# Optimization experiments

Measured on AMD Instinct MI355X. Metric: run time of the kernel, lower is better.

The kernel has to match this reference:

```python
import jax, jax.numpy as jnp
import numpy as np

N = 50000
E = 800000
D_IN = 128
D_HID = 256


def setup_inputs() -> dict:
    key = jax.random.key(0)
    ks = jax.random.split(key, 9)
    x = jax.random.normal(ks[0], (N, D_IN), dtype=jnp.float32)
    edge_index = jax.random.randint(ks[1], (2, E), 0, N, dtype=jnp.int64)
    edge_weight = jax.random.uniform(ks[2], (E,), dtype=jnp.float32)
    # GCNConv params (lin: y = x @ W.T, plus bias added after aggregation)
    W1 = jax.random.normal(ks[3], (D_HID, D_IN), dtype=jnp.float32) / np.sqrt(D_IN)
    b1 = jnp.zeros((D_HID,), dtype=jnp.float32)
    W2 = jax.random.normal(ks[4], (D_IN, D_HID), dtype=jnp.float32) / np.sqrt(D_HID)
    b2 = jnp.zeros((D_IN,), dtype=jnp.float32)
    gamma = jnp.ones((D_IN,), dtype=jnp.float32)
    beta = jnp.zeros((D_IN,), dtype=jnp.float32)
    return {"x": x, "edge_index": edge_index, "edge_weight": edge_weight,
            "W1": W1, "b1": b1, "W2": W2, "b2": b2,
            "gamma": gamma, "beta": beta}


def _gcn_norm(edge_index, edge_weight, n_nodes):
    # add self loops with weight 1.0 (PyG gcn_norm default)
    loop = jnp.arange(n_nodes, dtype=edge_index.dtype)
    src = jnp.concatenate([edge_index[0], loop])
    dst = jnp.concatenate([edge_index[1], loop])
    w = jnp.concatenate([edge_weight, jnp.ones((n_nodes,), edge_weight.dtype)])
    # symmetric normalization: deg over target index
    deg = jax.ops.segment_sum(w, dst, num_segments=n_nodes)
    dinv = jnp.where(deg > 0, jax.lax.rsqrt(deg), 0.0)
    norm = dinv[src] * w * dinv[dst]
    return src, dst, norm


def _gcn_conv(x, src, dst, norm, W, b, n_nodes):
    h = x @ W.T                                    # [N, out]
    msg = h[src] * norm[:, None]                   # gather + scale [E+N, out]
    out = jax.ops.segment_sum(msg, dst, num_segments=n_nodes)
    return out + b


def reference(x, edge_index, edge_weight, W1, b1, W2, b2, gamma, beta):
    n_nodes = x.shape[0]
    src, dst, norm = _gcn_norm(edge_index, edge_weight, n_nodes)
    h = _gcn_conv(x, src, dst, norm, W1, b1, n_nodes)
    h = jax.nn.relu(h)
    h = _gcn_conv(h, src, dst, norm, W2, b2, n_nodes)
    # LayerNorm over last dim
    mu = jnp.mean(h, axis=-1, keepdims=True)
    var = jnp.mean(jnp.square(h - mu), axis=-1, keepdims=True)
    h = (h - mu) * jax.lax.rsqrt(var + 1e-5) * gamma + beta
    return h
```

## Files before the change

### kernel.cpp

```cpp
#include <hip/hip_runtime.h>

typedef unsigned short ushort_t;
typedef __attribute__((ext_vector_type(8))) short short8;
typedef __attribute__((ext_vector_type(4))) float float4v;

#define MAXDEG 48
#define CSTRIDE 16

__device__ inline float b2f(ushort_t u) {
    unsigned x = ((unsigned)u) << 16;
    return __builtin_bit_cast(float, x);
}
__device__ inline ushort_t f2b(float f) {
    unsigned x = __builtin_bit_cast(unsigned, f);
    unsigned r = (x + 0x7fffu + ((x >> 16) & 1u)) >> 16;
    return (ushort_t)r;
}

__device__ inline void load_edge(const int* __restrict__ ei, int e, int E,
                                 int& s, int& d) {
    int ec = min(e, E - 1);
    int2 c64 = ((const int2*)ei)[ec];
    unsigned long long m = __ballot(c64.y != 0);
    if (m != 0ull) {
        s = ei[ec];
        d = ei[(size_t)E + ec];
    } else {
        s = c64.x;
        d = ((const int2*)ei)[(size_t)E + ec].x;
    }
}


__global__ __launch_bounds__(256) void k_mega(const int* __restrict__ ei,
                                              const float* __restrict__ w,
                                              const float* __restrict__ x,
                                              const float* __restrict__ W1,
                                              const float* __restrict__ W2,
                                              unsigned* packed,
                                              unsigned* __restrict__ edata,
                                              ushort_t* __restrict__ xb,
                                              ushort_t* __restrict__ W1b,
                                              ushort_t* __restrict__ W2b,
                                              int E, int Nn, int gE, int gX) {
    int b = blockIdx.x;
    if (b < gE) {
        int e = b * 256 + threadIdx.x;
        int s, d;
        load_edge(ei, e, E, s, d);
        if (e < E) {
            if ((unsigned)s < (unsigned)Nn && (unsigned)d < (unsigned)Nn) {
                float wv = w[e];
                unsigned fx = (unsigned)(wv * 65536.0f + 0.5f);
                unsigned old = atomicAdd(packed + (size_t)d * CSTRIDE,
                                         (1u << 22) | fx);
                int r = (int)(old >> 22);
                if (r < MAXDEG) {
                    unsigned wq = (unsigned)(wv * 32768.0f + 0.5f);
                    wq = min(wq, 32767u);
                    edata[(size_t)d * MAXDEG + r] = ((unsigned)s << 15) | wq;
                }
            }
        }
    } else if (b < gE + gX) {
        int i = (b - gE) * 256 + threadIdx.x;
        if (i < Nn * 32) {
            float4v v = ((const float4v*)x)[i];
            ushort4 o;
            o.x = f2b(v[0]); o.y = f2b(v[1]); o.z = f2b(v[2]); o.w = f2b(v[3]);
            ((ushort4*)xb)[i] = o;
        }
    } else {
        int i = (b - gE - gX) * 256 + threadIdx.x;
        if (i < 32768) W1b[i] = f2b(W1[i]);
        else if (i < 65536) W2b[i - 32768] = f2b(W2[i - 32768]);
    }
}


__global__ __launch_bounds__(256) void k_dinv(const unsigned* __restrict__ packed,
                                              float* __restrict__ dinv, int Nn) {
    int i = blockIdx.x * 256 + threadIdx.x;
    if (i < Nn) {
        float wsum = (float)(packed[(size_t)i * CSTRIDE] & 0x3FFFFFu) * (1.0f / 65536.0f);
        dinv[i] = rsqrtf(1.0f + wsum);
    }
}


__device__ inline void agg_edges(const ushort_t* __restrict__ src,
                                 const unsigned* __restrict__ ed, int n,
                                 const float* __restrict__ dinv,
                                 int hl, int p, float* a) {
    int i = 0;
    for (; i + 15 < n; i += 16) {
        unsigned e2[8];
#pragma unroll
        for (int j = 0; j < 8; ++j) e2[j] = ed[i + p + 2 * j];
        ushort4 q[8];
        float nw[8];
#pragma unroll
        for (int j = 0; j < 8; ++j) {
            int sN = (int)(e2[j] >> 15);
            q[j] = ((const ushort4*)(src + (size_t)sN * 128))[hl];
            nw[j] = dinv[sN] * (float)(e2[j] & 0x7FFFu) * (1.0f / 32768.0f);
        }
#pragma unroll
        for (int j = 0; j < 8; ++j) {
            a[0] += b2f(q[j].x) * nw[j]; a[1] += b2f(q[j].y) * nw[j];
            a[2] += b2f(q[j].z) * nw[j]; a[3] += b2f(q[j].w) * nw[j];
        }
    }
    for (; i + 7 < n; i += 8) {
        unsigned e2[4];
#pragma unroll
        for (int j = 0; j < 4; ++j) e2[j] = ed[i + p + 2 * j];
        ushort4 q[4];
        float nw[4];
#pragma unroll
        for (int j = 0; j < 4; ++j) {
            int sN = (int)(e2[j] >> 15);
            q[j] = ((const ushort4*)(src + (size_t)sN * 128))[hl];
            nw[j] = dinv[sN] * (float)(e2[j] & 0x7FFFu) * (1.0f / 32768.0f);
        }
#pragma unroll
        for (int j = 0; j < 4; ++j) {
            a[0] += b2f(q[j].x) * nw[j]; a[1] += b2f(q[j].y) * nw[j];
            a[2] += b2f(q[j].z) * nw[j]; a[3] += b2f(q[j].w) * nw[j];
        }
    }
    for (; i < n; i += 2) {
        int idx = i + p;
        int ic = min(idx, n - 1);
        unsigned e2 = ed[ic];
        int sN = (int)(e2 >> 15);
        float nw = (idx < n)
                       ? dinv[sN] * (float)(e2 & 0x7FFFu) * (1.0f / 32768.0f)
                       : 0.f;
        ushort4 q = ((const ushort4*)(src + (size_t)sN * 128))[hl];
        a[0] += b2f(q.x) * nw; a[1] += b2f(q.y) * nw;
        a[2] += b2f(q.z) * nw; a[3] += b2f(q.w) * nw;
    }
}


__global__ __launch_bounds__(256) void k_agg1(const ushort_t* __restrict__ xb,
                                              const unsigned* __restrict__ packed,
                                              const unsigned* __restrict__ edata,
                                              const float* __restrict__ dinv,
                                              ushort_t* __restrict__ ax, int Nn) {
    int v = (blockIdx.x * blockDim.x + threadIdx.x) >> 6;
    int lane = threadIdx.x & 63;
    if (v >= Nn) return;
    int hl = lane & 31, p = lane >> 5;
    float dv = dinv[v];
    float a[4] = {0.f, 0.f, 0.f, 0.f};
    if (p == 0) {
        ushort4 pq = ((const ushort4*)(xb + (size_t)v * 128))[hl];
        a[0] = b2f(pq.x) * dv; a[1] = b2f(pq.y) * dv;
        a[2] = b2f(pq.z) * dv; a[3] = b2f(pq.w) * dv;
    }
    int n = min((int)(packed[(size_t)v * CSTRIDE] >> 22), MAXDEG);
    agg_edges(xb, edata + (size_t)v * MAXDEG, n, dinv, hl, p, a);
#pragma unroll
    for (int j = 0; j < 4; ++j) {
        a[j] *= dv;
        a[j] += __shfl_xor(a[j], 32);
    }
    if (p == 0) {
        ushort4 o;
        o.x = f2b(a[0]); o.y = f2b(a[1]); o.z = f2b(a[2]); o.w = f2b(a[3]);
        ((ushort4*)(ax + (size_t)v * 128))[hl] = o;
    }
}


__global__ __launch_bounds__(256, 2) void k_gemm_fused(const ushort_t* __restrict__ ax,
                                                       const ushort_t* __restrict__ W1b,
                                                       const float* __restrict__ b1v,
                                                       const ushort_t* __restrict__ W2b,
                                                       ushort_t* __restrict__ h2, int Nn) {
    __shared__ ushort_t tile[64][264];
    int tid = threadIdx.x, wid = tid >> 6, lane = tid & 63;
    int m = lane & 15, q = lane >> 4;
    int blk = blockIdx.x * 64;

    short8 wf[4][4];
#pragma unroll
    for (int nt = 0; nt < 4; ++nt) {
        const ushort_t* wb = W1b + (size_t)(wid * 64 + nt * 16 + m) * 128 + q * 8;
#pragma unroll
        for (int kt = 0; kt < 4; ++kt) wf[nt][kt] = *(const short8*)(wb + kt * 32);
    }
    short8 af[4][4];
#pragma unroll
    for (int mi = 0; mi < 4; ++mi) {
        int arow = blk + mi * 16 + m;
        bool rv = arow < Nn;
        const ushort_t* ab = ax + (size_t)arow * 128 + q * 8;
#pragma unroll
        for (int kt = 0; kt < 4; ++kt)
            af[mi][kt] = rv ? *(const short8*)(ab + kt * 32) : (short8)0;
    }

    float4v acc1[4][4];
#pragma unroll
    for (int mi = 0; mi < 4; ++mi)
#pragma unroll
        for (int nt = 0; nt < 4; ++nt) acc1[mi][nt] = (float4v){0.f, 0.f, 0.f, 0.f};

#pragma unroll
    for (int kt = 0; kt < 4; ++kt)
#pragma unroll
        for (int mi = 0; mi < 4; ++mi)
#pragma unroll
            for (int nt = 0; nt < 4; ++nt)
                acc1[mi][nt] = __builtin_amdgcn_mfma_f32_16x16x32_bf16(
                    af[mi][kt], wf[nt][kt], acc1[mi][nt], 0, 0, 0);

#pragma unroll
    for (int nt = 0; nt < 4; ++nt) {
        int col = wid * 64 + nt * 16 + m;
        float bb = b1v[col];
#pragma unroll
        for (int mi = 0; mi < 4; ++mi) {
#pragma unroll
            for (int r = 0; r < 4; ++r) {
                float v = acc1[mi][nt][r] + bb;
                v = v > 0.f ? v : 0.f;
                tile[mi * 16 + q * 4 + r][col] = f2b(v);
            }
        }
    }
    __syncthreads();

    short8 w2f[2][8];
#pragma unroll
    for (int n2 = 0; n2 < 2; ++n2) {
        const ushort_t* wb = W2b + (size_t)(wid * 32 + n2 * 16 + m) * 256 + q * 8;
#pragma unroll
        for (int kt = 0; kt < 8; ++kt) w2f[n2][kt] = *(const short8*)(wb + kt * 32);
    }

    float4v acc2[4][2];
#pragma unroll
    for (int mi = 0; mi < 4; ++mi)
#pragma unroll
        for (int n2 = 0; n2 < 2; ++n2) acc2[mi][n2] = (float4v){0.f, 0.f, 0.f, 0.f};

#pragma unroll
    for (int kt = 0; kt < 8; ++kt) {
#pragma unroll
        for (int mi = 0; mi < 4; ++mi) {
            short8 a2 = *(const short8*)&tile[mi * 16 + m][kt * 32 + q * 8];
#pragma unroll
            for (int n2 = 0; n2 < 2; ++n2)
                acc2[mi][n2] = __builtin_amdgcn_mfma_f32_16x16x32_bf16(
                    a2, w2f[n2][kt], acc2[mi][n2], 0, 0, 0);
        }
    }

#pragma unroll
    for (int mi = 0; mi < 4; ++mi) {
#pragma unroll
        for (int n2 = 0; n2 < 2; ++n2) {
            int col = wid * 32 + n2 * 16 + m;
#pragma unroll
            for (int r = 0; r < 4; ++r) {
                int row = blk + mi * 16 + q * 4 + r;
                if (row < Nn) h2[(size_t)row * 128 + col] = f2b(acc2[mi][n2][r]);
            }
        }
    }
}


__global__ __launch_bounds__(256) void k_agg2_ln(const ushort_t* __restrict__ h2,
                                                 const unsigned* __restrict__ packed,
                                                 const unsigned* __restrict__ edata,
                                                 const float* __restrict__ dinv,
                                                 const float* __restrict__ b2v,
                                                 const float* __restrict__ gv,
                                                 const float* __restrict__ bev,
                                                 float* __restrict__ out, int Nn) {
    int v = (blockIdx.x * blockDim.x + threadIdx.x) >> 6;
    int lane = threadIdx.x & 63;
    if (v >= Nn) return;
    int hl = lane & 31, p = lane >> 5;
    float dv = dinv[v];
    float a[4] = {0.f, 0.f, 0.f, 0.f};
    if (p == 0) {
        ushort4 pq = ((const ushort4*)(h2 + (size_t)v * 128))[hl];
        a[0] = b2f(pq.x) * dv; a[1] = b2f(pq.y) * dv;
        a[2] = b2f(pq.z) * dv; a[3] = b2f(pq.w) * dv;
    }
    int n = min((int)(packed[(size_t)v * CSTRIDE] >> 22), MAXDEG);
    agg_edges(h2, edata + (size_t)v * MAXDEG, n, dinv, hl, p, a);
#pragma unroll
    for (int j = 0; j < 4; ++j) {
        a[j] *= dv;
        a[j] += __shfl_xor(a[j], 32);
    }

    int d0 = hl * 4;
#pragma unroll
    for (int j = 0; j < 4; ++j) a[j] += b2v[d0 + j];

    float ssum = a[0] + a[1] + a[2] + a[3];
    float ssq = a[0] * a[0] + a[1] * a[1] + a[2] * a[2] + a[3] * a[3];
#pragma unroll
    for (int off = 1; off < 64; off <<= 1) {
        ssum += __shfl_xor(ssum, off);
        ssq += __shfl_xor(ssq, off);
    }
    float mu = ssum * (1.0f / 256.0f);
    float var = ssq * (1.0f / 256.0f) - mu * mu;
    float r = rsqrtf(var + 1e-5f);
    if (p == 0) {
        float4v o;
#pragma unroll
        for (int j = 0; j < 4; ++j)
            o[j] = (a[j] - mu) * r * gv[d0 + j] + bev[d0 + j];
        ((float4v*)(out + (size_t)v * 128))[hl] = o;
    }
}


extern "C" void kernel_launch(void* const* d_in, const int* in_sizes, int n_in,
                              void* d_out, int out_size, void* d_ws, size_t ws_size,
                              hipStream_t stream) {
    const float* x   = (const float*)d_in[0];
    const int*   ei  = (const int*)d_in[1];
    const float* ew  = (const float*)d_in[2];
    const float* W1  = (const float*)d_in[3];
    const float* b1v = (const float*)d_in[4];
    const float* W2  = (const float*)d_in[5];
    const float* b2v = (const float*)d_in[6];
    const float* gv  = (const float*)d_in[7];
    const float* bev = (const float*)d_in[8];
    float* out = (float*)d_out;

    const int Nn = in_sizes[0] / 128;
    const int E  = in_sizes[2];

    char* base = (char*)d_ws;
    size_t off = 0;
    auto alloc = [&](size_t bytes) {
        char* p = base + off;
        off = (off + bytes + 255) & ~(size_t)255;
        return p;
    };
    unsigned* packed = (unsigned*)alloc((size_t)Nn * CSTRIDE * 4);
    float*    dinv   = (float*)alloc((size_t)Nn * 4);
    unsigned* edata  = (unsigned*)alloc((size_t)Nn * MAXDEG * 4);
    ushort_t* xb     = (ushort_t*)alloc((size_t)Nn * 128 * 2);
    ushort_t* h2     = (ushort_t*)alloc((size_t)Nn * 128 * 2);
    ushort_t* W1b    = (ushort_t*)alloc(32768 * 2);
    ushort_t* W2b    = (ushort_t*)alloc(32768 * 2);
    ushort_t* ax     = (ushort_t*)d_out;
    (void)ws_size; (void)n_in; (void)out_size;

    int gE = (E + 255) / 256;
    int gX = (Nn * 32 + 255) / 256;
    int gW = (Nn + 3) / 4;
    int gG = (Nn + 63) / 64;
    int gD = (Nn + 255) / 256;

    hipMemsetAsync(packed, 0, (size_t)Nn * CSTRIDE * 4, stream);
    k_mega<<<gE + gX + 256, 256, 0, stream>>>(ei, ew, x, W1, W2, packed, edata,
                                              xb, W1b, W2b, E, Nn, gE, gX);
    k_dinv<<<gD, 256, 0, stream>>>(packed, dinv, Nn);
    k_agg1<<<gW, 256, 0, stream>>>(xb, packed, edata, dinv, ax, Nn);
    k_gemm_fused<<<gG, 256, 0, stream>>>(ax, W1b, b1v, W2b, h2, Nn);
    k_agg2_ln<<<gW, 256, 0, stream>>>(h2, packed, edata, dinv, b2v, gv, bev, out, Nn);
}
```

Measured before the change: 244.4 us.

## Drop dinv kernel, compact packed counters, interleave edge and convert blocks

Removes the separate k_dinv launch and the dinv array; the aggregation kernels now recompute rsqrt(1+wsum) from the packed degree/weight word for each neighbour. The packed counter array loses its 16-word stride and becomes dense, shrinking the memset and making the gather of neighbour normalisation coalesced-friendlier. In k_mega, edge blocks are interleaved 1:2 with conversion blocks to spread atomic traffic across the grid. The trade is an extra rsqrt per edge, and more atomic contention on neighbouring counters that now share cache lines.

```diff
diff --git a/kernel.cpp b/kernel.cpp
--- a/kernel.cpp
+++ b/kernel.cpp
@@ -5,7 +5,6 @@
 typedef __attribute__((ext_vector_type(4))) float float4v;
 
 #define MAXDEG 48
-#define CSTRIDE 16
 
 __device__ inline float b2f(ushort_t u) {
     unsigned x = ((unsigned)u) << 16;
@@ -15,6 +14,9 @@
     unsigned x = __builtin_bit_cast(unsigned, f);
     unsigned r = (x + 0x7fffu + ((x >> 16) & 1u)) >> 16;
     return (ushort_t)r;
+}
+__device__ inline float pk2dinv(unsigned pk) {
+    return rsqrtf(1.0f + (float)(pk & 0x3FFFFFu) * (1.0f / 65536.0f));
 }
 
 __device__ inline void load_edge(const int* __restrict__ ei, int e, int E,
@@ -44,16 +46,29 @@
                                               ushort_t* __restrict__ W2b,
                                               int E, int Nn, int gE, int gX) {
     int b = blockIdx.x;
-    if (b < gE) {
-        int e = b * 256 + threadIdx.x;
+    bool isEdge;
+    int widx;
+    if (3 * gE <= (int)gridDim.x) {
+        if (b < 3 * gE) {
+            if (b % 3 == 0) { isEdge = true;  widx = b / 3; }
+            else            { isEdge = false; widx = b - b / 3 - 1; }
+        } else {
+            isEdge = false; widx = b - gE;
+        }
+    } else {
+        isEdge = b < gE;
+        widx = isEdge ? b : b - gE;
+    }
+
+    if (isEdge) {
+        int e = widx * 256 + threadIdx.x;
         int s, d;
         load_edge(ei, e, E, s, d);
         if (e < E) {
             if ((unsigned)s < (unsigned)Nn && (unsigned)d < (unsigned)Nn) {
                 float wv = w[e];
                 unsigned fx = (unsigned)(wv * 65536.0f + 0.5f);
-                unsigned old = atomicAdd(packed + (size_t)d * CSTRIDE,
-                                         (1u << 22) | fx);
+                unsigned old = atomicAdd(packed + d, (1u << 22) | fx);
                 int r = (int)(old >> 22);
                 if (r < MAXDEG) {
                     unsigned wq = (unsigned)(wv * 32768.0f + 0.5f);
@@ -62,8 +77,8 @@
                 }
             }
         }
-    } else if (b < gE + gX) {
-        int i = (b - gE) * 256 + threadIdx.x;
+    } else if (widx < gX) {
+        int i = widx * 256 + threadIdx.x;
         if (i < Nn * 32) {
             float4v v = ((const float4v*)x)[i];
             ushort4 o;
@@ -71,26 +86,16 @@
             ((ushort4*)xb)[i] = o;
         }
     } else {
-        int i = (b - gE - gX) * 256 + threadIdx.x;
+        int i = (widx - gX) * 256 + threadIdx.x;
         if (i < 32768) W1b[i] = f2b(W1[i]);
         else if (i < 65536) W2b[i - 32768] = f2b(W2[i - 32768]);
     }
 }
 
 
-__global__ __launch_bounds__(256) void k_dinv(const unsigned* __restrict__ packed,
-                                              float* __restrict__ dinv, int Nn) {
-    int i = blockIdx.x * 256 + threadIdx.x;
-    if (i < Nn) {
-        float wsum = (float)(packed[(size_t)i * CSTRIDE] & 0x3FFFFFu) * (1.0f / 65536.0f);
-        dinv[i] = rsqrtf(1.0f + wsum);
-    }
-}
-
-
 __device__ inline void agg_edges(const ushort_t* __restrict__ src,
                                  const unsigned* __restrict__ ed, int n,
-                                 const float* __restrict__ dinv,
+                                 const unsigned* __restrict__ packed,
                                  int hl, int p, float* a) {
     int i = 0;
     for (; i + 15 < n; i += 16) {
@@ -103,7 +108,7 @@
         for (int j = 0; j < 8; ++j) {
             int sN = (int)(e2[j] >> 15);
             q[j] = ((const ushort4*)(src + (size_t)sN * 128))[hl];
-            nw[j] = dinv[sN] * (float)(e2[j] & 0x7FFFu) * (1.0f / 32768.0f);
+            nw[j] = pk2dinv(packed[sN]) * (float)(e2[j] & 0x7FFFu) * (1.0f / 32768.0f);
         }
 #pragma unroll
         for (int j = 0; j < 8; ++j) {
@@ -121,7 +126,7 @@
         for (int j = 0; j < 4; ++j) {
             int sN = (int)(e2[j] >> 15);
             q[j] = ((const ushort4*)(src + (size_t)sN * 128))[hl];
-            nw[j] = dinv[sN] * (float)(e2[j] & 0x7FFFu) * (1.0f / 32768.0f);
+            nw[j] = pk2dinv(packed[sN]) * (float)(e2[j] & 0x7FFFu) * (1.0f / 32768.0f);
         }
 #pragma unroll
         for (int j = 0; j < 4; ++j) {
@@ -135,7 +140,7 @@
         unsigned e2 = ed[ic];
         int sN = (int)(e2 >> 15);
         float nw = (idx < n)
-                       ? dinv[sN] * (float)(e2 & 0x7FFFu) * (1.0f / 32768.0f)
+                       ? pk2dinv(packed[sN]) * (float)(e2 & 0x7FFFu) * (1.0f / 32768.0f)
                        : 0.f;
         ushort4 q = ((const ushort4*)(src + (size_t)sN * 128))[hl];
         a[0] += b2f(q.x) * nw; a[1] += b2f(q.y) * nw;
@@ -147,21 +152,21 @@
 __global__ __launch_bounds__(256) void k_agg1(const ushort_t* __restrict__ xb,
                                               const unsigned* __restrict__ packed,
                                               const unsigned* __restrict__ edata,
-                                              const float* __restrict__ dinv,
                                               ushort_t* __restrict__ ax, int Nn) {
     int v = (blockIdx.x * blockDim.x + threadIdx.x) >> 6;
     int lane = threadIdx.x & 63;
     if (v >= Nn) return;
     int hl = lane & 31, p = lane >> 5;
-    float dv = dinv[v];
+    unsigned pk = packed[v];
+    float dv = pk2dinv(pk);
     float a[4] = {0.f, 0.f, 0.f, 0.f};
     if (p == 0) {
         ushort4 pq = ((const ushort4*)(xb + (size_t)v * 128))[hl];
         a[0] = b2f(pq.x) * dv; a[1] = b2f(pq.y) * dv;
         a[2] = b2f(pq.z) * dv; a[3] = b2f(pq.w) * dv;
     }
-    int n = min((int)(packed[(size_t)v * CSTRIDE] >> 22), MAXDEG);
-    agg_edges(xb, edata + (size_t)v * MAXDEG, n, dinv, hl, p, a);
+    int n = min((int)(pk >> 22), MAXDEG);
+    agg_edges(xb, edata + (size_t)v * MAXDEG, n, packed, hl, p, a);
 #pragma unroll
     for (int j = 0; j < 4; ++j) {
         a[j] *= dv;
@@ -278,7 +283,6 @@
 __global__ __launch_bounds__(256) void k_agg2_ln(const ushort_t* __restrict__ h2,
                                                  const unsigned* __restrict__ packed,
                                                  const unsigned* __restrict__ edata,
-                                                 const float* __restrict__ dinv,
                                                  const float* __restrict__ b2v,
                                                  const float* __restrict__ gv,
                                                  const float* __restrict__ bev,
@@ -287,15 +291,16 @@
     int lane = threadIdx.x & 63;
     if (v >= Nn) return;
     int hl = lane & 31, p = lane >> 5;
-    float dv = dinv[v];
+    unsigned pk = packed[v];
+    float dv = pk2dinv(pk);
     float a[4] = {0.f, 0.f, 0.f, 0.f};
     if (p == 0) {
         ushort4 pq = ((const ushort4*)(h2 + (size_t)v * 128))[hl];
         a[0] = b2f(pq.x) * dv; a[1] = b2f(pq.y) * dv;
         a[2] = b2f(pq.z) * dv; a[3] = b2f(pq.w) * dv;
     }
-    int n = min((int)(packed[(size_t)v * CSTRIDE] >> 22), MAXDEG);
-    agg_edges(h2, edata + (size_t)v * MAXDEG, n, dinv, hl, p, a);
+    int n = min((int)(pk >> 22), MAXDEG);
+    agg_edges(h2, edata + (size_t)v * MAXDEG, n, packed, hl, p, a);
 #pragma unroll
     for (int j = 0; j < 4; ++j) {
         a[j] *= dv;
@@ -350,8 +355,7 @@
         off = (off + bytes + 255) & ~(size_t)255;
         return p;
     };
-    unsigned* packed = (unsigned*)alloc((size_t)Nn * CSTRIDE * 4);
-    float*    dinv   = (float*)alloc((size_t)Nn * 4);
+    unsigned* packed = (unsigned*)alloc((size_t)Nn * 4);
     unsigned* edata  = (unsigned*)alloc((size_t)Nn * MAXDEG * 4);
     ushort_t* xb     = (ushort_t*)alloc((size_t)Nn * 128 * 2);
     ushort_t* h2     = (ushort_t*)alloc((size_t)Nn * 128 * 2);
@@ -365,12 +369,12 @@
     int gW = (Nn + 3) / 4;
     int gG = (Nn + 63) / 64;
     int gD = (Nn + 255) / 256;
-
-    hipMemsetAsync(packed, 0, (size_t)Nn * CSTRIDE * 4, stream);
+    (void)gD;
+
+    hipMemsetAsync(packed, 0, (size_t)Nn * 4, stream);
     k_mega<<<gE + gX + 256, 256, 0, stream>>>(ei, ew, x, W1, W2, packed, edata,
                                               xb, W1b, W2b, E, Nn, gE, gX);
-    k_dinv<<<gD, 256, 0, stream>>>(packed, dinv, Nn);
-    k_agg1<<<gW, 256, 0, stream>>>(xb, packed, edata, dinv, ax, Nn);
+    k_agg1<<<gW, 256, 0, stream>>>(xb, packed, edata, ax, Nn);
     k_gemm_fused<<<gG, 256, 0, stream>>>(ax, W1b, b1v, W2b, h2, Nn);
-    k_agg2_ln<<<gW, 256, 0, stream>>>(h2, packed, edata, dinv, b2v, gv, bev, out, Nn);
-}
+    k_agg2_ln<<<gW, 256, 0, stream>>>(h2, packed, edata, b2v, gv, bev, out, Nn);
+}
```

New measurement: 257.8 us. +5.5%, slower.

## Pack per-node atomic counters densely and interleave edge blocks with conversion blocks

Applied to the files above, without the earlier changes.

Removes the 16-word padding stride on the per-node packed degree/weight counters, so the memset and later reads touch a 16x smaller array. The edge-bucketing blocks are also interleaved one-in-three with the x/weight bf16 conversion blocks, so atomic-heavy and streaming work share the machine at once instead of running as separate phases. Dense counters can raise same-cache-line atomic contention between neighbouring nodes, trading less memory traffic for more collisions.

```diff
diff --git a/kernel.cpp b/kernel.cpp
--- a/kernel.cpp
+++ b/kernel.cpp
@@ -5,7 +5,6 @@
 typedef __attribute__((ext_vector_type(4))) float float4v;
 
 #define MAXDEG 48
-#define CSTRIDE 16
 
 __device__ inline float b2f(ushort_t u) {
     unsigned x = ((unsigned)u) << 16;
@@ -44,16 +43,29 @@
                                               ushort_t* __restrict__ W2b,
                                               int E, int Nn, int gE, int gX) {
     int b = blockIdx.x;
-    if (b < gE) {
-        int e = b * 256 + threadIdx.x;
+    bool isEdge;
+    int widx;
+    if (3 * gE <= (int)gridDim.x) {
+        if (b < 3 * gE) {
+            if (b % 3 == 0) { isEdge = true;  widx = b / 3; }
+            else            { isEdge = false; widx = b - b / 3 - 1; }
+        } else {
+            isEdge = false; widx = b - gE;
+        }
+    } else {
+        isEdge = b < gE;
+        widx = isEdge ? b : b - gE;
+    }
+
+    if (isEdge) {
+        int e = widx * 256 + threadIdx.x;
         int s, d;
         load_edge(ei, e, E, s, d);
         if (e < E) {
             if ((unsigned)s < (unsigned)Nn && (unsigned)d < (unsigned)Nn) {
                 float wv = w[e];
                 unsigned fx = (unsigned)(wv * 65536.0f + 0.5f);
-                unsigned old = atomicAdd(packed + (size_t)d * CSTRIDE,
-                                         (1u << 22) | fx);
+                unsigned old = atomicAdd(packed + d, (1u << 22) | fx);
                 int r = (int)(old >> 22);
                 if (r < MAXDEG) {
                     unsigned wq = (unsigned)(wv * 32768.0f + 0.5f);
@@ -62,8 +74,8 @@
                 }
             }
         }
-    } else if (b < gE + gX) {
-        int i = (b - gE) * 256 + threadIdx.x;
+    } else if (widx < gX) {
+        int i = widx * 256 + threadIdx.x;
         if (i < Nn * 32) {
             float4v v = ((const float4v*)x)[i];
             ushort4 o;
@@ -71,7 +83,7 @@
             ((ushort4*)xb)[i] = o;
         }
     } else {
-        int i = (b - gE - gX) * 256 + threadIdx.x;
+        int i = (widx - gX) * 256 + threadIdx.x;
         if (i < 32768) W1b[i] = f2b(W1[i]);
         else if (i < 65536) W2b[i - 32768] = f2b(W2[i - 32768]);
     }
@@ -82,7 +94,7 @@
                                               float* __restrict__ dinv, int Nn) {
     int i = blockIdx.x * 256 + threadIdx.x;
     if (i < Nn) {
-        float wsum = (float)(packed[(size_t)i * CSTRIDE] & 0x3FFFFFu) * (1.0f / 65536.0f);
+        float wsum = (float)(packed[i] & 0x3FFFFFu) * (1.0f / 65536.0f);
         dinv[i] = rsqrtf(1.0f + wsum);
     }
 }
@@ -160,7 +172,7 @@
         a[0] = b2f(pq.x) * dv; a[1] = b2f(pq.y) * dv;
         a[2] = b2f(pq.z) * dv; a[3] = b2f(pq.w) * dv;
     }
-    int n = min((int)(packed[(size_t)v * CSTRIDE] >> 22), MAXDEG);
+    int n = min((int)(packed[v] >> 22), MAXDEG);
     agg_edges(xb, edata + (size_t)v * MAXDEG, n, dinv, hl, p, a);
 #pragma unroll
     for (int j = 0; j < 4; ++j) {
@@ -294,7 +306,7 @@
         a[0] = b2f(pq.x) * dv; a[1] = b2f(pq.y) * dv;
         a[2] = b2f(pq.z) * dv; a[3] = b2f(pq.w) * dv;
     }
-    int n = min((int)(packed[(size_t)v * CSTRIDE] >> 22), MAXDEG);
+    int n = min((int)(packed[v] >> 22), MAXDEG);
     agg_edges(h2, edata + (size_t)v * MAXDEG, n, dinv, hl, p, a);
 #pragma unroll
     for (int j = 0; j < 4; ++j) {
@@ -350,7 +362,7 @@
         off = (off + bytes + 255) & ~(size_t)255;
         return p;
     };
-    unsigned* packed = (unsigned*)alloc((size_t)Nn * CSTRIDE * 4);
+    unsigned* packed = (unsigned*)alloc((size_t)Nn * 4);
     float*    dinv   = (float*)alloc((size_t)Nn * 4);
     unsigned* edata  = (unsigned*)alloc((size_t)Nn * MAXDEG * 4);
     ushort_t* xb     = (ushort_t*)alloc((size_t)Nn * 128 * 2);
@@ -366,7 +378,7 @@
     int gG = (Nn + 63) / 64;
     int gD = (Nn + 255) / 256;
 
-    hipMemsetAsync(packed, 0, (size_t)Nn * CSTRIDE * 4, stream);
+    hipMemsetAsync(packed, 0, (size_t)Nn * 4, stream);
     k_mega<<<gE + gX + 256, 256, 0, stream>>>(ei, ew, x, W1, W2, packed, edata,
                                               xb, W1b, W2b, E, Nn, gE, gX);
     k_dinv<<<gD, 256, 0, stream>>>(packed, dinv, Nn);
```

Result: no change. 243.4 us (-0.4%).
